# Performance work log

Measured on AMD Instinct MI355X. Metric: run time of the kernel, lower is better.

The kernel has to match this reference:

```python
import jax, jax.numpy as jnp
import numpy as np

B, T, DIM = 2, 2048, 1040
H = 16
HD = (DIM - 1) // H  # 64 spatial dims per head; per-head width = HD + 1
EPS = 1e-6


def _rotary_tables(seq_len, dtype):
    inv_freq = 1.0 / (10000.0 ** (jnp.arange(0, HD, 2, dtype=jnp.float32) / (HD - 2 * EPS)))
    t = jnp.arange(seq_len, dtype=jnp.float32)
    freqs = jnp.outer(t, inv_freq)  # [T, HD//2]
    cos = jnp.cos(freqs).astype(dtype)[None, :, None, :]  # [1,T,1,HD//2]
    sin = jnp.sin(freqs).astype(dtype)[None, :, None, :]
    return cos, sin


def _apply_hyp_rotary(x, cos, sin):
    # x: [B,T,H,HD+1]; component 0 is the Lorentz time coordinate
    x_sp = x[..., 1:]
    d = x_sp.shape[-1] // 2
    x1, x2 = x_sp[..., :d], x_sp[..., d:]
    y1 = x1 * cos + x2 * sin
    y2 = -x1 * sin + x2 * cos
    rot = jnp.clip(jnp.concatenate([y1, y2], axis=-1), -1000.0, 1000.0)
    sp_sq = jnp.clip(jnp.sum(rot * rot, axis=-1, keepdims=True), 0.0, 1e6)
    new_x0 = jnp.sqrt(1.0 + sp_sq + EPS)  # re-project onto hyperboloid
    return jnp.concatenate([new_x0, rot], axis=-1)


def setup_inputs() -> dict:
    key = jax.random.key(0)
    kx, kq, kk, kv, kp = jax.random.split(key, 5)
    scale = 0.02  # xavier_normal gain 0.02 in the original
    x = jax.random.normal(kx, (B, T, DIM), dtype=jnp.float32)
    Wq = jax.random.normal(kq, (DIM, DIM), dtype=jnp.float32) * scale
    Wk = jax.random.normal(kk, (DIM, DIM), dtype=jnp.float32) * scale
    Wv = jax.random.normal(kv, (DIM, DIM), dtype=jnp.float32) * scale
    Wp = jax.random.normal(kp, (DIM, DIM), dtype=jnp.float32) * scale
    return {"x": x, "Wq": Wq, "Wk": Wk, "Wv": Wv, "Wp": Wp}


def reference(x, Wq, Wk, Wv, Wp):
    b, t, _ = x.shape
    q = (x @ Wq.T).reshape(b, t, H, HD + 1)
    k = (x @ Wk.T).reshape(b, t, H, HD + 1)
    v = (x @ Wv.T).reshape(b, t, H, HD + 1)
    cos, sin = _rotary_tables(t, x.dtype)
    q = _apply_hyp_rotary(q, cos, sin)
    k = _apply_hyp_rotary(k, cos, sin)
    # Lorentzian inner product scores: -q0*k0 + <q_sp, k_sp>
    spatial = jnp.einsum('bthd,bshd->bhts', q[..., 1:], k[..., 1:])
    lorentz = jnp.einsum('bth,bsh->bhts', q[..., 0], k[..., 0])
    logits = jnp.clip((spatial - lorentz) / (HD ** 0.5), -100.0, 100.0)
    attn = jax.nn.softmax(logits, axis=-1)
    y = jnp.einsum('bhts,bshd->bthd', attn, v).reshape(b, t, DIM)
    return y @ Wp.T
```

## Files before the change

### kernel.cpp

```cpp
#include <hip/hip_runtime.h>
#include <math.h>

#define B_   2
#define T_   2048
#define DIM_ 1040
#define H_   16
#define HD_  64
#define HD1_ 65
#define NELEM (B_*T_*DIM_)

#define KP_   1056
#define NP_   1152
#define NP3_  3456
#define SEGS_ 132
#define MROWS_ (B_*T_)

#define NBH_  (B_*H_)
#define VTR_  72
#define QKW_  96

#define PR_A_ (NP3_*SEGS_)
#define PR_B_ (PR_A_ + MROWS_*SEGS_)
#define PR_C_ (PR_B_ + NBH_*7*256)
#define PR_D_ (PR_C_ + NP_*SEGS_)

typedef __attribute__((ext_vector_type(8))) __bf16 bf16x8;
typedef __attribute__((ext_vector_type(4))) float f32x4;
typedef __attribute__((ext_vector_type(8))) unsigned short ushort8;

static __device__ __forceinline__ unsigned pack_bf16(float lo, float hi) {
    __bf16 a = (__bf16)lo, c = (__bf16)hi;
    unsigned short ua, uc;
    __builtin_memcpy(&ua, &a, 2);
    __builtin_memcpy(&uc, &c, 2);
    return ((unsigned)uc << 16) | ua;
}

static __device__ __forceinline__ float exp2_fast(float x) {
    float r;
    asm("v_exp_f32 %0, %1" : "=v"(r) : "v"(x));
    return r;
}

static __device__ __forceinline__ void conv_row_plain(
    const float* __restrict__ in, __bf16* __restrict__ out, int r, int s,
    int rows_in)
{
    float v[8];
    if (r < rows_in && s < 130) {
        const float4 f0 = *(const float4*)(in + (size_t)r * DIM_ + s * 8);
        const float4 f1 = *(const float4*)(in + (size_t)r * DIM_ + s * 8 + 4);
        v[0]=f0.x; v[1]=f0.y; v[2]=f0.z; v[3]=f0.w;
        v[4]=f1.x; v[5]=f1.y; v[6]=f1.z; v[7]=f1.w;
    } else {
        #pragma unroll
        for (int i = 0; i < 8; ++i) v[i] = 0.0f;
    }
    __bf16 t[8] __attribute__((aligned(16)));
    #pragma unroll
    for (int i = 0; i < 8; ++i) t[i] = (__bf16)v[i];
    *(ushort8*)(out) = *(const ushort8*)(t);
}

__global__ __launch_bounds__(256)
void prep_all(const float* __restrict__ x,  const float* __restrict__ Wq,
              const float* __restrict__ Wk, const float* __restrict__ Wv,
              const float* __restrict__ Wp, __bf16* __restrict__ xb,
              __bf16* __restrict__ Wb3, __bf16* __restrict__ VT,
              __bf16* __restrict__ WpB)
{
    const int gid = blockIdx.x * 256 + threadIdx.x;
    if (gid < PR_A_) {
        const int r = gid / SEGS_, s = gid - r * SEGS_;
        const int seg = r / NP_, rr = r - seg * NP_;
        const float* in = (seg == 0) ? Wq : (seg == 1) ? Wk : Wv;
        conv_row_plain(in, Wb3 + (size_t)r * KP_ + s * 8, rr, s, DIM_);
    } else if (gid < PR_B_) {
        const int g = gid - PR_A_;
        const int r = g / SEGS_, s = g - r * SEGS_;
        conv_row_plain(x, xb + (size_t)r * KP_ + s * 8, r, s, MROWS_);
    } else if (gid < PR_C_) {
        const int cid = gid - PR_B_;
        const int bh  = cid / 1792;
        const int rem = cid - bh * 1792;
        const int row = 65 + rem / 256;
        const int tc  = rem - (row - 65) * 256;
        const unsigned val = (row == 65) ? 0x3F803F80u : 0u;
        unsigned* p = (unsigned*)(VT + ((size_t)bh * VTR_ + row) * T_ + tc * 8);
        p[0] = val; p[1] = val; p[2] = val; p[3] = val;
    } else {
        const int g = gid - PR_C_;
        const int r = g / SEGS_, s = g - r * SEGS_;
        conv_row_plain(Wp, WpB + (size_t)r * KP_ + s * 8, r, s, DIM_);
    }
}

__device__ __forceinline__ void gload_lds16(const void* g, void* l) {
    __builtin_amdgcn_global_load_lds(
        (const __attribute__((address_space(1))) void*)g,
        (__attribute__((address_space(3))) void*)l, 16, 0, 0);
}

#define GEMM_PURE_CORE(Ac_, Bw_, N0_, M0_)                                    \
    __shared__ __bf16 As[128 * 96];                                           \
    __shared__ __bf16 Bs[128 * 96];                                           \
    const int tid  = threadIdx.x;                                             \
    const int lane = tid & 63;                                                \
    const int w    = tid >> 6;                                                \
    const int wr   = (w >> 1) * 64, wc = (w & 1) * 64;                        \
    const __bf16* gap[6]; const __bf16* gb[6];                                \
    _Pragma("unroll")                                                         \
    for (int qi = 0; qi < 6; ++qi) {                                          \
        const int cid = qi * 256 + tid;                                       \
        const int rr  = cid / 12, cc = cid - rr * 12;                         \
        gap[qi] = Ac_ + (size_t)(M0_ + rr) * KP_ + cc * 8;                    \
        gb[qi]  = Bw_ + (size_t)(N0_ + rr) * KP_ + cc * 8;                    \
    }                                                                         \
    f32x4 acc[4][4];                                                          \
    _Pragma("unroll")                                                         \
    for (int i = 0; i < 4; ++i)                                               \
        _Pragma("unroll")                                                     \
        for (int j = 0; j < 4; ++j) acc[i][j] = (f32x4){0.f, 0.f, 0.f, 0.f};  \
    const __bf16* pa = As + (wr + (lane & 15)) * 96 + (lane >> 4) * 8;        \
    const __bf16* pb = Bs + (wc + (lane & 15)) * 96 + (lane >> 4) * 8;        \
    for (int k0 = 0; k0 < KP_; k0 += 96) {                                    \
        __syncthreads();                                                      \
        _Pragma("unroll")                                                     \
        for (int qi = 0; qi < 6; ++qi) {                                      \
            gload_lds16(gap[qi] + k0, As + (qi * 256 + tid) * 8);             \
            gload_lds16(gb[qi]  + k0, Bs + (qi * 256 + tid) * 8);             \
        }                                                                     \
        __syncthreads();                                                      \
        _Pragma("unroll")                                                     \
        for (int ks = 0; ks < 3; ++ks) {                                      \
            bf16x8 a[4], b[4];                                                \
            _Pragma("unroll")                                                 \
            for (int i = 0; i < 4; ++i)                                       \
                a[i] = *(const bf16x8*)(pa + i * 16 * 96 + ks * 32);          \
            _Pragma("unroll")                                                 \
            for (int j = 0; j < 4; ++j)                                       \
                b[j] = *(const bf16x8*)(pb + j * 16 * 96 + ks * 32);          \
            __builtin_amdgcn_s_setprio(1);                                    \
            _Pragma("unroll")                                                 \
            for (int i = 0; i < 4; ++i)                                       \
                _Pragma("unroll")                                             \
                for (int j = 0; j < 4; ++j)                                   \
                    acc[i][j] = __builtin_amdgcn_mfma_f32_16x16x32_bf16(      \
                        a[i], b[j], acc[i][j], 0, 0, 0);                      \
            __builtin_amdgcn_s_setprio(0);                                    \
        }                                                                     \
    }

__global__ __launch_bounds__(256)
void gemm_qkv_b(const __bf16* __restrict__ Ac, const __bf16* __restrict__ Bw,
                float* __restrict__ Cq, float* __restrict__ Ck,
                __bf16* __restrict__ VTout)
{
    const int bid = blockIdx.x;
    const int gid = (bid & 7) * 108 + (bid >> 3);
    const int n0  = (gid >> 5) * 128;
    const int m0  = (gid & 31) * 128;
    GEMM_PURE_CORE(Ac, Bw, n0, m0)

    const int seg = n0 / NP_;
    const int rbase = m0 + wr + (lane >> 4) * 4;
    const int cbase = n0 - seg * NP_ + wc + (lane & 15);

    if (seg < 2) {
        float* C = seg ? Ck : Cq;
        #pragma unroll
        for (int i = 0; i < 4; ++i)
            #pragma unroll
            for (int j = 0; j < 4; ++j) {
                const int n = cbase + j * 16;
                if (n < DIM_) {
                    #pragma unroll
                    for (int r = 0; r < 4; ++r)
                        C[(size_t)(rbase + i * 16 + r) * DIM_ + n] = acc[i][j][r];
                }
            }
    } else {
        #pragma unroll
        for (int i = 0; i < 4; ++i) {
            const int tg = rbase + i * 16;
            const int bb = tg >> 11, tt = tg & (T_ - 1);
            #pragma unroll
            for (int j = 0; j < 4; ++j) {
                const int n = cbase + j * 16;
                if (n < DIM_) {
                    const int h = n / 65, d = n - h * 65;
                    const size_t off =
                        ((size_t)(bb * H_ + h) * VTR_ + d) * T_ + tt;
                    uint2 pk;
                    pk.x = pack_bf16(acc[i][j][0], acc[i][j][1]);
                    pk.y = pack_bf16(acc[i][j][2], acc[i][j][3]);
                    *(uint2*)(VTout + off) = pk;
                }
            }
        }
    }
}

__global__ __launch_bounds__(256)
void gemm_out_b(const __bf16* __restrict__ Ac, const __bf16* __restrict__ Bw,
                float* __restrict__ C)
{
    const int bid = blockIdx.x;
    const int gid = (bid & 7) * 36 + (bid >> 3);
    const int n0  = (gid >> 5) * 128;
    const int m0  = (gid & 31) * 128;
    GEMM_PURE_CORE(Ac, Bw, n0, m0)

    const int rbase = m0 + wr + (lane >> 4) * 4;
    const int cbase = n0 + wc + (lane & 15);
    #pragma unroll
    for (int i = 0; i < 4; ++i)
        #pragma unroll
        for (int j = 0; j < 4; ++j) {
            const int n = cbase + j * 16;
            if (n < DIM_) {
                #pragma unroll
                for (int r = 0; r < 4; ++r)
                    C[(size_t)(rbase + i * 16 + r) * DIM_ + n] = acc[i][j][r];
            }
        }
}

__global__ __launch_bounds__(256)
void rotary2(const float* __restrict__ Xq, const float* __restrict__ Xk,
             __bf16* __restrict__ QB, __bf16* __restrict__ KB)
{
    const int gwid = (blockIdx.x * 256 + threadIdx.x) >> 6;
    const int lane = threadIdx.x & 63;
    const int which = gwid >> 16;
    const int wid   = gwid & 65535;

    const float SCALE = 0.18033688f;

    const int h  = wid & (H_ - 1);
    const int bt = wid >> 4;
    const int t  = bt & (T_ - 1);
    const int b  = bt >> 11;
    const float* base = (which ? Xk : Xq) + (size_t)bt * DIM_ + h * HD1_;

    const int j = lane & 31;
    const float pw = powf(10000.0f, (float)j * (1.0f / 32.0f));
    const float fr = (float)t * (1.0f / pw);
    const float cs = cosf(fr);
    const float sn = sinf(fr);

    const float x1 = base[1 + j];
    const float x2 = base[33 + j];

    float rot = (lane < 32) ? (x1 * cs + x2 * sn)
                            : (x2 * cs - x1 * sn);
    rot = fminf(fmaxf(rot, -1000.0f), 1000.0f);

    float sq = rot * rot;
    #pragma unroll
    for (int off = 32; off >= 1; off >>= 1)
        sq += __shfl_xor(sq, off, 64);
    sq = fminf(fmaxf(sq, 0.0f), 1.0e6f);

    const float x0 = sqrtf((1.0f + sq) + 1.0e-6f);

    __bf16* XB = which ? KB : QB;
    const size_t base96 = (size_t)((b * H_ + h) * T_ + t) * QKW_;
    XB[base96 + lane] = which ? (__bf16)rot : (__bf16)(SCALE * rot);

    if (lane < 32) {
        float v = 0.0f;
        const float d0 = x0 - 5.25f;
        if (which) {
            const float bh = (float)(__bf16)d0;
            if (lane == 0 || lane == 2) v = bh;
            else if (lane == 1) v = d0 - bh;
        } else {
            if (lane < 2) v = -SCALE * 5.25f;
            else if (lane == 2) v = -SCALE * (float)(__bf16)d0;
        }
        XB[base96 + 64 + lane] = (__bf16)v;
    }
}

__global__ __launch_bounds__(256)
void attn_mfma7(const __bf16* __restrict__ QB, const __bf16* __restrict__ KB,
                const __bf16* __restrict__ VT, __bf16* __restrict__ yb)
{
    __shared__ __bf16 Kt[2][64 * 96] __attribute__((aligned(16)));
    __shared__ __bf16 Vt[80 * 64] __attribute__((aligned(16)));
    __shared__ __bf16 Pt[64 * 72] __attribute__((aligned(16)));

    const int tid  = threadIdx.x;
    const int lane = tid & 63;
    const int w    = tid >> 6;
    const int lx   = lane & 15;
    const int ly   = lane >> 4;
    const int bh   = blockIdx.x;
    const int q0r  = blockIdx.y * 64;

    const __bf16* QBb = QB + (size_t)bh * T_ * QKW_;
    const __bf16* KBb = KB + (size_t)bh * T_ * QKW_;
    const __bf16* VTb = VT + (size_t)bh * VTR_ * T_;

    bf16x8 aq[3];
    #pragma unroll
    for (int ks = 0; ks < 3; ++ks)
        aq[ks] = *(const bf16x8*)
            (QBb + (size_t)(q0r + w * 16 + lx) * QKW_ + ks * 32 + ly * 8);

    ((unsigned*)Vt)[2304 + tid] = 0u;

    int offk[3];
    #pragma unroll
    for (int qi = 0; qi < 3; ++qi) {
        const int cid = qi * 256 + tid;
        const int s = cid / 12, p = cid - s * 12;
        const int c = (p & 12) | ((p - (s >> 1)) & 3);
        offk[qi] = s * QKW_ + c * 8;
    }
    int offv[3];
    #pragma unroll
    for (int qi = 0; qi < 3; ++qi) {
        const int cid = qi * 256 + tid;
        const int d = cid >> 3, jj = cid & 7;
        offv[qi] = d * T_ + (jj ^ (d & 7)) * 8;
    }

    #pragma unroll
    for (int qi = 0; qi < 3; ++qi)
        gload_lds16(KBb + offk[qi], &Kt[0][(qi * 256 + tid) * 8]);

    f32x4 acc_o[5];
    #pragma unroll
    for (int n = 0; n < 5; ++n) acc_o[n] = (f32x4){0.f, 0.f, 0.f, 0.f};

    const int rr = (ly + (lx >> 1)) & 3;

    int cur = 0;
    for (int it = 0; it < T_ / 64; ++it) {
        const int s0 = it * 64;
        __syncthreads();

        gload_lds16(VTb + s0 + offv[0], Vt + tid * 8);
        gload_lds16(VTb + s0 + offv[1], Vt + (256 + tid) * 8);
        if (tid < 64)
            gload_lds16(VTb + s0 + offv[2], Vt + (512 + tid) * 8);

        if (it + 1 < T_ / 64) {
            const int koff = (s0 + 64) * QKW_;
            #pragma unroll
            for (int qi = 0; qi < 3; ++qi)
                gload_lds16(KBb + koff + offk[qi],
                            &Kt[cur ^ 1][(qi * 256 + tid) * 8]);
        }

        f32x4 sc[4];
        __builtin_amdgcn_s_setprio(1);
        #pragma unroll
        for (int n = 0; n < 4; ++n) {
            f32x4 c = (f32x4){0.f, 0.f, 0.f, 0.f};
            #pragma unroll
            for (int ks = 0; ks < 3; ++ks) {
                const bf16x8 bk = *(const bf16x8*)
                    &Kt[cur][(n * 16 + lx) * 96 + ks * 32 + rr * 8];
                c = __builtin_amdgcn_mfma_f32_16x16x32_bf16(
                    aq[ks], bk, c, 0, 0, 0);
            }
            sc[n] = c;
        }
        __builtin_amdgcn_s_setprio(0);

        #pragma unroll
        for (int n = 0; n < 4; ++n)
            #pragma unroll
            for (int r = 0; r < 4; ++r)
                Pt[(w * 16 + ly * 4 + r) * 72 + n * 16 + lx] =
                    (__bf16)exp2_fast(sc[n][r]);

        __syncthreads();

        bf16x8 ap[2];
        #pragma unroll
        for (int ks = 0; ks < 2; ++ks)
            ap[ks] = *(const bf16x8*)
                &Pt[(w * 16 + lx) * 72 + ks * 32 + ly * 8];
        __builtin_amdgcn_s_setprio(1);
        #pragma unroll
        for (int n = 0; n < 5; ++n) {
            f32x4 c = acc_o[n];
            #pragma unroll
            for (int ks = 0; ks < 2; ++ks) {
                const bf16x8 bv = *(const bf16x8*)
                    &Vt[(n * 16 + lx) * 64 + ((ks * 4 + ly) ^ (lx & 7)) * 8];
                c = __builtin_amdgcn_mfma_f32_16x16x32_bf16(
                    ap[ks], bv, c, 0, 0, 0);
            }
            acc_o[n] = c;
        }
        __builtin_amdgcn_s_setprio(0);
        cur ^= 1;
    }

    const int b = bh >> 4, h = bh & 15;
    #pragma unroll
    for (int r = 0; r < 4; ++r) {
        const float l = __shfl(acc_o[4][r], (lane & 48) + 1, 64);
        const float inv = 1.0f / l;
        const int qrow = q0r + w * 16 + ly * 4 + r;
        __bf16* yrow = yb + (size_t)(b * T_ + qrow) * KP_ + h * HD1_;
        #pragma unroll
        for (int n = 0; n < 4; ++n)
            yrow[n * 16 + lx] = (__bf16)(acc_o[n][r] * inv);
        if (lx == 0) yrow[64] = (__bf16)(acc_o[4][r] * inv);
    }
}

extern "C" void kernel_launch(void* const* d_in, const int* in_sizes, int n_in,
                              void* d_out, int out_size, void* d_ws, size_t ws_size,
                              hipStream_t stream)
{
    const float* x  = (const float*)d_in[0];
    const float* Wq = (const float*)d_in[1];
    const float* Wk = (const float*)d_in[2];
    const float* Wv = (const float*)d_in[3];
    const float* Wp = (const float*)d_in[4];

    float*  q   = (float*)d_ws;
    float*  k   = q + NELEM;
    __bf16* xb  = (__bf16*)(k + NELEM);
    __bf16* Wb3 = xb + (size_t)MROWS_ * KP_;
    __bf16* QB  = Wb3 + (size_t)NP3_ * KP_;
    __bf16* KB  = QB + (size_t)NBH_ * T_ * QKW_;
    __bf16* VT  = KB + (size_t)NBH_ * T_ * QKW_;
    __bf16* WpB = VT + (size_t)NBH_ * VTR_ * T_;
    __bf16* yb  = xb;

    float* out = (float*)d_out;

    dim3 blk(256);

    prep_all<<<dim3(PR_D_ / 256), blk, 0, stream>>>(
        x, Wq, Wk, Wv, Wp, xb, Wb3, VT, WpB);
    gemm_qkv_b<<<dim3(864), blk, 0, stream>>>(xb, Wb3, q, k, VT);

    rotary2<<<dim3(2 * (B_ * T_ * H_) / 4), blk, 0, stream>>>(q, k, QB, KB);

    attn_mfma7<<<dim3(NBH_, T_ / 64), blk, 0, stream>>>(QB, KB, VT, yb);

    gemm_out_b<<<dim3(288), blk, 0, stream>>>(yb, WpB, out);
}
```

Measured before the change: 230.3 us.

## Split attention over key halves with separate reduction kernel

```diff
diff --git a/kernel.cpp b/kernel.cpp
--- a/kernel.cpp
+++ b/kernel.cpp
@@ -284,8 +284,9 @@
 }
 
 __global__ __launch_bounds__(256)
-void attn_mfma7(const __bf16* __restrict__ QB, const __bf16* __restrict__ KB,
-                const __bf16* __restrict__ VT, __bf16* __restrict__ yb)
+void attn_mfma8(const __bf16* __restrict__ QB, const __bf16* __restrict__ KB,
+                const __bf16* __restrict__ VT, float* __restrict__ Op,
+                float* __restrict__ lp)
 {
     __shared__ __bf16 Kt[2][64 * 96] __attribute__((aligned(16)));
     __shared__ __bf16 Vt[80 * 64] __attribute__((aligned(16)));
@@ -298,6 +299,8 @@
     const int ly   = lane >> 4;
     const int bh   = blockIdx.x;
     const int q0r  = blockIdx.y * 64;
+    const int half = blockIdx.z;
+    const int sbase = half * (T_ / 2);
 
     const __bf16* QBb = QB + (size_t)bh * T_ * QKW_;
     const __bf16* KBb = KB + (size_t)bh * T_ * QKW_;
@@ -329,7 +332,8 @@
 
     #pragma unroll
     for (int qi = 0; qi < 3; ++qi)
-        gload_lds16(KBb + offk[qi], &Kt[0][(qi * 256 + tid) * 8]);
+        gload_lds16(KBb + (size_t)sbase * QKW_ + offk[qi],
+                    &Kt[0][(qi * 256 + tid) * 8]);
 
     f32x4 acc_o[5];
     #pragma unroll
@@ -338,8 +342,8 @@
     const int rr = (ly + (lx >> 1)) & 3;
 
     int cur = 0;
-    for (int it = 0; it < T_ / 64; ++it) {
-        const int s0 = it * 64;
+    for (int it = 0; it < T_ / 128; ++it) {
+        const int s0 = sbase + it * 64;
         __syncthreads();
 
         gload_lds16(VTb + s0 + offv[0], Vt + tid * 8);
@@ -347,8 +351,8 @@
         if (tid < 64)
             gload_lds16(VTb + s0 + offv[2], Vt + (512 + tid) * 8);
 
-        if (it + 1 < T_ / 64) {
-            const int koff = (s0 + 64) * QKW_;
+        if (it + 1 < T_ / 128) {
+            const size_t koff = (size_t)(s0 + 64) * QKW_;
             #pragma unroll
             for (int qi = 0; qi < 3; ++qi)
                 gload_lds16(KBb + koff + offk[qi],
@@ -402,17 +406,41 @@
         cur ^= 1;
     }
 
+    float* Oh = Op + (size_t)half * NELEM;
+    float* lh = lp + (size_t)half * NBH_ * T_;
+    #pragma unroll
+    for (int r = 0; r < 4; ++r) {
+        const int qrow = q0r + w * 16 + ly * 4 + r;
+        float* orow = Oh + ((size_t)bh * T_ + qrow) * 65;
+        #pragma unroll
+        for (int n = 0; n < 4; ++n)
+            orow[n * 16 + lx] = acc_o[n][r];
+        if (lx == 0) orow[64] = acc_o[4][r];
+        if (lx == 1) lh[(size_t)bh * T_ + qrow] = acc_o[4][r];
+    }
+}
+
+__global__ __launch_bounds__(256)
+void attn_reduce(const float* __restrict__ Op, const float* __restrict__ lp,
+                 __bf16* __restrict__ yb)
+{
+    const int gwid = (blockIdx.x * 256 + threadIdx.x) >> 6;
+    const int lane = threadIdx.x & 63;
+    const int bh = gwid >> 11, t = gwid & (T_ - 1);
+    const size_t row = (size_t)bh * T_ + t;
+    const size_t r0 = row * 65;
+
+    const float l = lp[row] + lp[(size_t)NBH_ * T_ + row];
+    const float inv = 1.0f / l;
+
     const int b = bh >> 4, h = bh & 15;
-    #pragma unroll
-    for (int r = 0; r < 4; ++r) {
-        const float l = __shfl(acc_o[4][r], (lane & 48) + 1, 64);
-        const float inv = 1.0f / l;
-        const int qrow = q0r + w * 16 + ly * 4 + r;
-        __bf16* yrow = yb + (size_t)(b * T_ + qrow) * KP_ + h * HD1_;
-        #pragma unroll
-        for (int n = 0; n < 4; ++n)
-            yrow[n * 16 + lx] = (__bf16)(acc_o[n][r] * inv);
-        if (lx == 0) yrow[64] = (__bf16)(acc_o[4][r] * inv);
+    __bf16* yrow = yb + (size_t)(b * T_ + t) * KP_ + h * HD1_;
+
+    const float v = Op[r0 + lane] + Op[(size_t)NELEM + r0 + lane];
+    yrow[lane] = (__bf16)(v * inv);
+    if (lane == 0) {
+        const float v2 = Op[r0 + 64] + Op[(size_t)NELEM + r0 + 64];
+        yrow[64] = (__bf16)(v2 * inv);
     }
 }
 
@@ -434,6 +462,8 @@
     __bf16* KB  = QB + (size_t)NBH_ * T_ * QKW_;
     __bf16* VT  = KB + (size_t)NBH_ * T_ * QKW_;
     __bf16* WpB = VT + (size_t)NBH_ * VTR_ * T_;
+    float*  lp  = (float*)(WpB + (size_t)NP_ * KP_);
+    float*  Op  = q;
     __bf16* yb  = xb;
 
     float* out = (float*)d_out;
@@ -446,7 +476,8 @@
 
     rotary2<<<dim3(2 * (B_ * T_ * H_) / 4), blk, 0, stream>>>(q, k, QB, KB);
 
-    attn_mfma7<<<dim3(NBH_, T_ / 64), blk, 0, stream>>>(QB, KB, VT, yb);
+    attn_mfma8<<<dim3(NBH_, T_ / 64, 2), blk, 0, stream>>>(QB, KB, VT, Op, lp);
+    attn_reduce<<<dim3(NBH_ * T_ / 4), blk, 0, stream>>>(Op, lp, yb);
 
     gemm_out_b<<<dim3(288), blk, 0, stream>>>(yb, WpB, out);
 }
```

Result: no change. 233.7 us (+1.5%).
